# Performance work log

Hardware: AMD Instinct MI355X
Metric: run time of the kernel (lower is better)

Reference implementation:

```python
import jax, jax.numpy as jnp
import numpy as np

N_NODES = 50000
N_EDGES = 800000
N_RELS = 20
N_BASES = 8


def setup_inputs() -> dict:
    key = jax.random.key(0)
    ks = jax.random.split(key, 12)
    s = 0.05  # keep activations well-scaled through summed messages
    return {
        "src": jax.random.randint(ks[0], (N_EDGES,), 0, N_NODES),
        "dst": jax.random.randint(ks[1], (N_EDGES,), 0, N_NODES),
        "etype": jax.random.randint(ks[2], (N_EDGES,), 0, N_RELS),
        "num_nodes": N_NODES,
        "basis0": jax.random.normal(ks[3], (N_BASES, 1, 128), jnp.float32) * s,
        "wcomp0": jax.random.normal(ks[4], (N_RELS, N_BASES), jnp.float32),
        "bias0": jax.random.normal(ks[5], (128,), jnp.float32) * s,
        "basis1": jax.random.normal(ks[6], (N_BASES, 128, 128), jnp.float32) * s,
        "wcomp1": jax.random.normal(ks[7], (N_RELS, N_BASES), jnp.float32),
        "bias1": jax.random.normal(ks[8], (128,), jnp.float32) * s,
        "lin_w": jax.random.normal(ks[9], (128, 64), jnp.float32) * s,
        "lin_b": jax.random.normal(ks[10], (64,), jnp.float32) * s,
    }


def _relgraphconv(h, basis, w_comp, bias, src, dst, etype, num_nodes, relu):
    # Basis decomposition: W[r] = sum_b w_comp[r,b] * basis[b]  -> [R, in, out]
    W = jnp.einsum("rb,bio->rio", w_comp, basis)
    # Project every node under every relation once: [N, R, out]
    proj = jnp.einsum("ni,rio->nro", h, W)
    # Per-edge message = h[src] @ W[etype]  (gather, irregular access)
    msg = proj[src, etype]                       # [E, out]
    # Sum-aggregate messages into destination nodes (DGL fn.sum)
    agg = jax.ops.segment_sum(msg, dst, num_segments=num_nodes)
    out = agg + bias
    return jax.nn.relu(out) if relu else out


def reference(src, dst, etype, num_nodes, basis0, wcomp0, bias0,
              basis1, wcomp1, bias1, lin_w, lin_b):
    # Embedder.forward: h starts as ones [N, 1]
    h = jnp.ones((num_nodes, 1), jnp.float32)
    h = _relgraphconv(h, basis0, wcomp0, bias0, src, dst, etype, num_nodes, True)
    h = _relgraphconv(h, basis1, wcomp1, bias1, src, dst, etype, num_nodes, True)
    # conv_output=False -> final layer is plain Linear
    return h @ lin_w + lin_b
```

## Files before the change

### kernel.cpp

```cpp
#include <hip/hip_runtime.h>
#include <hip/hip_bf16.h>

#define NN 50000
#define NE 800000
#define NR 20
#define NB 8
#define D  128
#define DO 64
#define NT 782
#define NBKT (NT*1280)
#define NSB 978

typedef __attribute__((ext_vector_type(8))) short short8;
typedef __attribute__((ext_vector_type(4))) float f32x4;

__device__ inline unsigned short f2bf(float f) {
    __hip_bfloat16 h = __float2bfloat16(f);
    return *reinterpret_cast<unsigned short*>(&h);
}
__device__ inline float bf2f(unsigned short u) {
    unsigned x = ((unsigned)u) << 16;
    float f;
    __builtin_memcpy(&f, &x, 4);
    return f;
}


__global__ __launch_bounds__(1024) void k_wh(
        const float* __restrict__ basis0, const float* __restrict__ wcomp0,
        const float* __restrict__ basis1, const float* __restrict__ wcomp1,
        const float* __restrict__ lin_w,
        const int* __restrict__ dst, const int* __restrict__ et,
        float* __restrict__ W0, unsigned short* __restrict__ W1b,
        unsigned short* __restrict__ linWb, int* __restrict__ cnt2) {
    int b = blockIdx.x;
    if (b < 40) {
        int idx = b * 1024 + threadIdx.x;
        if (idx < NR * D) {
            int r = idx / D, o = idx % D;
            float a = 0.f;
            #pragma unroll
            for (int bb = 0; bb < NB; bb++) a += wcomp0[r * NB + bb] * basis0[bb * D + o];
            W0[idx] = a;
        }
        if (idx < 16 * 64) {
            int lane = idx & 63, fr = idx >> 6;
            int kc = fr >> 2, nt = fr & 3;
            int i0 = kc * 32 + (lane >> 4) * 8;
            int o = nt * 16 + (lane & 15);
            short8 v;
            #pragma unroll
            for (int e = 0; e < 8; e++) v[e] = (short)f2bf(lin_w[(i0 + e) * DO + o]);
            *((short8*)linWb + idx) = v;
        }
        {
            int lane = idx & 63;
            int cb   = (idx >> 6) & 7;
            int kc   = (idx >> 9) & 3;
            int rel  = idx >> 11;
            float wc[NB];
            #pragma unroll
            for (int bb = 0; bb < NB; bb++) wc[bb] = wcomp1[rel * NB + bb];
            int o  = cb * 16 + (lane & 15);
            int i0 = kc * 32 + (lane >> 4) * 8;
            short8 v;
            #pragma unroll
            for (int e = 0; e < 8; e++) {
                int i = i0 + e;
                float a = 0.f;
                #pragma unroll
                for (int bb = 0; bb < NB; bb++) a += wc[bb] * basis1[(bb * D + i) * D + o];
                v[e] = (short)f2bf(a);
            }
            *((short8*)W1b + idx) = v;
        }
    } else {
        int i = (b - 40) * 1024 + threadIdx.x;
        if (i < NE) {
            int d = dst[i];
            int key = (d >> 6) * 1280 + et[i] * 64 + (d & 63);
            atomicAdd(&cnt2[key], 1);
        }
    }
}

__global__ __launch_bounds__(1024) void k_scan1(const int* __restrict__ cnt2,
                                                int* __restrict__ boff2,
                                                int* __restrict__ bsum,
                                                int* __restrict__ scancnt) {
    __shared__ int ws[16];
    __shared__ int lastf;
    int t = threadIdx.x, lane = t & 63, wv = t >> 6;
    int i = blockIdx.x * 1024 + t;
    int v = (i < NBKT) ? cnt2[i] : 0;
    int inc = v;
    for (int dd = 1; dd < 64; dd <<= 1) {
        int u = __shfl_up(inc, dd);
        if (lane >= dd) inc += u;
    }
    if (lane == 63) ws[wv] = inc;
    __syncthreads();
    if (t == 0) { int a = 0; for (int j = 0; j < 16; j++) { int x = ws[j]; ws[j] = a; a += x; } }
    __syncthreads();
    int ex = ws[wv] + inc - v;
    if (i < NBKT) boff2[i] = ex;
    if (t == 1023) {
        bsum[blockIdx.x] = ex + v;
        __threadfence();
        int done = atomicAdd(scancnt, 1);
        lastf = (done == (int)gridDim.x - 1);
    }
    __syncthreads();
    if (!lastf) return;
    int v2 = (t < NSB) ? atomicAdd(&bsum[t], 0) : 0;
    int inc2 = v2;
    for (int dd = 1; dd < 64; dd <<= 1) {
        int u = __shfl_up(inc2, dd);
        if (lane >= dd) inc2 += u;
    }
    __syncthreads();
    if (lane == 63) ws[wv] = inc2;
    __syncthreads();
    if (t == 0) { int a = 0; for (int j = 0; j < 16; j++) { int x = ws[j]; ws[j] = a; a += x; } }
    __syncthreads();
    if (t < NSB) bsum[t] = ws[wv] + inc2 - v2;
}

__global__ __launch_bounds__(1024) void k_mid(
        int* __restrict__ boff2, const int* __restrict__ bsum,
        int* __restrict__ gcur2, const int* __restrict__ cnt2,
        const float* __restrict__ W0, const float* __restrict__ bias0,
        unsigned short* __restrict__ h1b) {
    __shared__ float cs[NR * 64];
    __shared__ float w0s[NR * D];
    int t = threadIdx.x, b = blockIdx.x;
    int i = b * 1024 + t;
    if (i < NBKT) {
        int f = boff2[i] + bsum[i >> 10];
        boff2[i] = f;
        gcur2[i] = f;
    }
    if (i == 0) boff2[NBKT] = NE;
    if (b < NT) {
        for (int j = t; j < NR * 64; j += 1024) cs[j] = (float)cnt2[b * 1280 + j];
        for (int j = t; j < NR * D; j += 1024) w0s[j] = W0[j];
        __syncthreads();
        int nl = t >> 4, cg = t & 15;
        int n = b * 64 + nl;
        if (n < NN) {
            float a[8];
            #pragma unroll
            for (int j = 0; j < 8; j++) a[j] = bias0[cg * 8 + j];
            for (int r = 0; r < NR; r++) {
                float c = cs[r * 64 + nl];
                #pragma unroll
                for (int j = 0; j < 8; j++) a[j] += c * w0s[r * D + cg * 8 + j];
            }
            short8 o;
            #pragma unroll
            for (int j = 0; j < 8; j++) o[j] = (short)f2bf(fmaxf(a[j], 0.f));
            *((short8*)(h1b + n * D + cg * 8)) = o;
        }
    }
}

__global__ __launch_bounds__(1024) void k_scatter(
        const int* __restrict__ src, const int* __restrict__ dst,
        const int* __restrict__ et, int* __restrict__ gcur2,
        unsigned short* __restrict__ epack) {
    int i = blockIdx.x * 1024 + threadIdx.x;
    if (i < NE) {
        int d = dst[i];
        int key = (d >> 6) * 1280 + et[i] * 64 + (d & 63);
        int pos = atomicAdd(&gcur2[key], 1);
        epack[pos] = (unsigned short)src[i];
    }
}

__global__ __launch_bounds__(512, 2) void k_mega(
        const unsigned short* __restrict__ epack, const int* __restrict__ boff2,
        const unsigned short* __restrict__ h1b,
        const unsigned short* __restrict__ W1b,
        const unsigned short* __restrict__ linWb,
        const float* __restrict__ bias1, const float* __restrict__ lin_b,
        float* __restrict__ out) {
    __shared__ __align__(16) char lds[17408 + 16384];
    __shared__ unsigned short ooffs[1282];
    __shared__ unsigned short epk[2048];

    short8* Raw8 = (short8*)lds;
    short8* Sl8  = (short8*)(lds + 17408);

    int t = threadIdx.x, tile = blockIdx.x;
    int wv = t >> 6, lane = t & 63;
    int le = t >> 3, lp = t & 7;
    int dl = t >> 3, cg = t & 7;
    int row = lane & 15, gg = lane >> 4;

    int kbase = tile * 1280;
    int tb = boff2[kbase];
    for (int i = t; i < 1281; i += 512)
        ooffs[i] = (unsigned short)(boff2[kbase + i] - tb);
    __syncthreads();
    int nE = min((int)ooffs[1280], 2048);
    for (int i = t; i < nE; i += 512) epk[i] = epack[tb + i];
    __syncthreads();

    f32x4 acc[4];
    #pragma unroll
    for (int j = 0; j < 4; j++) acc[j] = (f32x4){0.f, 0.f, 0.f, 0.f};

    for (int r = 0; r < NR; r++) {
        int rbase = ooffs[r * 64];
        int cnt = ooffs[r * 64 + 64] - rbase;
        if (cnt == 0) continue;

        const short8* Wg8 = (const short8*)W1b + r * 2048;
        short8 breg[4];
        #pragma unroll
        for (int kc = 0; kc < 4; kc++) breg[kc] = Wg8[(kc * 8 + wv) * 64 + lane];

        float s[16];
        #pragma unroll
        for (int k = 0; k < 16; k++) s[k] = 0.f;
        int o0 = ooffs[r * 64 + dl] - rbase;
        int o1 = ooffs[r * 64 + dl + 1] - rbase;
        int nc = (cnt + 63) >> 6;

        for (int c = 0; c < nc; c++) {
            int cb0 = c * 64, m = min(64, cnt - cb0);
            if (c > 0) __syncthreads();
            if (le < m) {
                int node = epk[rbase + cb0 + le];
                const short8* hp = (const short8*)(h1b + (size_t)node * D) + lp * 2;
                Raw8[le * 17 + lp * 2]     = hp[0];
                Raw8[le * 17 + lp * 2 + 1] = hp[1];
            }
            __syncthreads();
            int lo = max(o0 - cb0, 0), hi = min(o1 - cb0, m);
            for (int p = lo; p < hi; p++) {
                short8 w0 = Raw8[p * 17 + 2 * cg];
                short8 w1 = Raw8[p * 17 + 2 * cg + 1];
                #pragma unroll
                for (int k = 0; k < 8; k++) {
                    s[k]     += bf2f((unsigned short)w0[k]);
                    s[8 + k] += bf2f((unsigned short)w1[k]);
                }
            }
        }
        short8 p0, p1;
        #pragma unroll
        for (int k = 0; k < 8; k++) {
            p0[k] = (short)f2bf(s[k]);
            p1[k] = (short)f2bf(s[8 + k]);
        }
        Sl8[dl * 16 + ((cg * 2)     ^ (dl & 15))] = p0;
        Sl8[dl * 16 + ((cg * 2 + 1) ^ (dl & 15))] = p1;
        __syncthreads();
        #pragma unroll
        for (int rb = 0; rb < 4; rb++) {
            int arow = rb * 16 + row;
            #pragma unroll
            for (int kc = 0; kc < 4; kc++) {
                short8 a = Sl8[arow * 16 + ((kc * 4 + gg) ^ (arow & 15))];
                acc[rb] = __builtin_amdgcn_mfma_f32_16x16x32_bf16(a, breg[kc], acc[rb], 0, 0, 0);
            }
        }
    }

    __syncthreads();
    unsigned short* Af = (unsigned short*)lds;
    #pragma unroll
    for (int rb = 0; rb < 4; rb++) {
        #pragma unroll
        for (int reg = 0; reg < 4; reg++) {
            int rr = rb * 16 + gg * 4 + reg;
            int col = wv * 16 + row;
            Af[rr * 136 + col] = f2bf(fmaxf(acc[rb][reg] + bias1[col], 0.f));
        }
    }
    __syncthreads();
    {
        int rb = wv & 3;
        int nt0 = (wv >> 2) * 2, nt1 = nt0 + 1;
        f32x4 ao0 = (f32x4){0.f, 0.f, 0.f, 0.f};
        f32x4 ao1 = (f32x4){0.f, 0.f, 0.f, 0.f};
        #pragma unroll
        for (int kc = 0; kc < 4; kc++) {
            short8 a = *(const short8*)(Af + (rb * 16 + row) * 136 + kc * 32 + gg * 8);
            short8 b0 = *((const short8*)linWb + (kc * 4 + nt0) * 64 + lane);
            short8 b1 = *((const short8*)linWb + (kc * 4 + nt1) * 64 + lane);
            ao0 = __builtin_amdgcn_mfma_f32_16x16x32_bf16(a, b0, ao0, 0, 0, 0);
            ao1 = __builtin_amdgcn_mfma_f32_16x16x32_bf16(a, b1, ao1, 0, 0, 0);
        }
        float lb0 = lin_b[nt0 * 16 + row];
        float lb1 = lin_b[nt1 * 16 + row];
        #pragma unroll
        for (int reg = 0; reg < 4; reg++) {
            int d = tile * 64 + rb * 16 + gg * 4 + reg;
            if (d < NN) {
                out[d * DO + nt0 * 16 + row] = ao0[reg] + lb0;
                out[d * DO + nt1 * 16 + row] = ao1[reg] + lb1;
            }
        }
    }
}

extern "C" void kernel_launch(void* const* d_in, const int* in_sizes, int n_in,
                              void* d_out, int out_size, void* d_ws, size_t ws_size,
                              hipStream_t stream) {
    const int*   src    = (const int*)d_in[0];
    const int*   dst    = (const int*)d_in[1];
    const int*   et     = (const int*)d_in[2];
    const float* basis0 = (const float*)d_in[4];
    const float* wcomp0 = (const float*)d_in[5];
    const float* bias0  = (const float*)d_in[6];
    const float* basis1 = (const float*)d_in[7];
    const float* wcomp1 = (const float*)d_in[8];
    const float* bias1  = (const float*)d_in[9];
    const float* lin_w  = (const float*)d_in[10];
    const float* lin_b  = (const float*)d_in[11];
    float* out = (float*)d_out;

    char* ws = (char*)d_ws;
    int*            cnt2    = (int*)           (ws + 0);
    int*            bsum    = (int*)           (ws + 4003840);
    int*            scancnt = (int*)           (ws + 4007752);
    int*            boff2   = (int*)           (ws + 4007808);
    int*            gcur2   = (int*)           (ws + 8011712);
    float*          W0      = (float*)         (ws + 12015616);
    unsigned short* W1b     = (unsigned short*)(ws + 12025856);
    unsigned short* h1b     = (unsigned short*)(ws + 12681216);
    unsigned short* epack   = (unsigned short*)(ws + 25481216);
    unsigned short* linWb   = (unsigned short*)(ws + 28681216);

    hipMemsetAsync(ws, 0, 4007756, stream);

    k_wh<<<NT + 40, 1024, 0, stream>>>(basis0, wcomp0, basis1, wcomp1, lin_w,
                                       dst, et, W0, W1b, linWb, cnt2);
    k_scan1<<<NSB, 1024, 0, stream>>>(cnt2, boff2, bsum, scancnt);
    k_mid<<<NSB, 1024, 0, stream>>>(boff2, bsum, gcur2, cnt2, W0, bias0, h1b);
    k_scatter<<<NT, 1024, 0, stream>>>(src, dst, et, gcur2, epack);
    k_mega<<<NT, 512, 0, stream>>>(epack, boff2, h1b, W1b, linWb,
                                   bias1, lin_b, out);
}
```

Before: 212.0 us.

## Split decoupled scan into separate kernels and fuse layer-0 compute with scatter

Replaces the last-block-done scan (atomic counter plus threadfence) with three kernels: a block-local scan, a single-block scan of the block sums, and an offset-fixup kernel. The layer-0 node feature computation moves from the fixup kernel into the scatter kernel as extra blocks, so it runs alongside the edge scatter. The edge-count blocks are reordered ahead of the weight-prep blocks in the first kernel. This removes the atomic and fence synchronisation but adds one kernel launch.

```diff
diff --git a/kernel.cpp b/kernel.cpp
--- a/kernel.cpp
+++ b/kernel.cpp
@@ -27,69 +27,67 @@
 
 
 __global__ __launch_bounds__(1024) void k_wh(
+        const int* __restrict__ dst, const int* __restrict__ et,
         const float* __restrict__ basis0, const float* __restrict__ wcomp0,
         const float* __restrict__ basis1, const float* __restrict__ wcomp1,
         const float* __restrict__ lin_w,
-        const int* __restrict__ dst, const int* __restrict__ et,
-        float* __restrict__ W0, unsigned short* __restrict__ W1b,
-        unsigned short* __restrict__ linWb, int* __restrict__ cnt2) {
+        int* __restrict__ cnt2, float* __restrict__ W0,
+        unsigned short* __restrict__ W1b, unsigned short* __restrict__ linWb) {
     int b = blockIdx.x;
-    if (b < 40) {
-        int idx = b * 1024 + threadIdx.x;
-        if (idx < NR * D) {
-            int r = idx / D, o = idx % D;
-            float a = 0.f;
-            #pragma unroll
-            for (int bb = 0; bb < NB; bb++) a += wcomp0[r * NB + bb] * basis0[bb * D + o];
-            W0[idx] = a;
-        }
-        if (idx < 16 * 64) {
-            int lane = idx & 63, fr = idx >> 6;
-            int kc = fr >> 2, nt = fr & 3;
-            int i0 = kc * 32 + (lane >> 4) * 8;
-            int o = nt * 16 + (lane & 15);
-            short8 v;
-            #pragma unroll
-            for (int e = 0; e < 8; e++) v[e] = (short)f2bf(lin_w[(i0 + e) * DO + o]);
-            *((short8*)linWb + idx) = v;
-        }
-        {
-            int lane = idx & 63;
-            int cb   = (idx >> 6) & 7;
-            int kc   = (idx >> 9) & 3;
-            int rel  = idx >> 11;
-            float wc[NB];
-            #pragma unroll
-            for (int bb = 0; bb < NB; bb++) wc[bb] = wcomp1[rel * NB + bb];
-            int o  = cb * 16 + (lane & 15);
-            int i0 = kc * 32 + (lane >> 4) * 8;
-            short8 v;
-            #pragma unroll
-            for (int e = 0; e < 8; e++) {
-                int i = i0 + e;
-                float a = 0.f;
-                #pragma unroll
-                for (int bb = 0; bb < NB; bb++) a += wc[bb] * basis1[(bb * D + i) * D + o];
-                v[e] = (short)f2bf(a);
-            }
-            *((short8*)W1b + idx) = v;
-        }
-    } else {
-        int i = (b - 40) * 1024 + threadIdx.x;
+    if (b < NT) {
+        int i = b * 1024 + threadIdx.x;
         if (i < NE) {
             int d = dst[i];
             int key = (d >> 6) * 1280 + et[i] * 64 + (d & 63);
             atomicAdd(&cnt2[key], 1);
         }
+        return;
+    }
+    int idx = (b - NT) * 1024 + threadIdx.x;
+    if (idx < NR * D) {
+        int r = idx / D, o = idx % D;
+        float a = 0.f;
+        #pragma unroll
+        for (int bb = 0; bb < NB; bb++) a += wcomp0[r * NB + bb] * basis0[bb * D + o];
+        W0[idx] = a;
+    }
+    if (idx < 16 * 64) {
+        int lane = idx & 63, fr = idx >> 6;
+        int kc = fr >> 2, nt = fr & 3;
+        int i0 = kc * 32 + (lane >> 4) * 8;
+        int o = nt * 16 + (lane & 15);
+        short8 v;
+        #pragma unroll
+        for (int e = 0; e < 8; e++) v[e] = (short)f2bf(lin_w[(i0 + e) * DO + o]);
+        *((short8*)linWb + idx) = v;
+    }
+    if (idx < NR * 4 * 8 * 64) {
+        int lane = idx & 63;
+        int cb   = (idx >> 6) & 7;
+        int kc   = (idx >> 9) & 3;
+        int rel  = idx >> 11;
+        float wc[NB];
+        #pragma unroll
+        for (int bb = 0; bb < NB; bb++) wc[bb] = wcomp1[rel * NB + bb];
+        int o  = cb * 16 + (lane & 15);
+        int i0 = kc * 32 + (lane >> 4) * 8;
+        short8 v;
+        #pragma unroll
+        for (int e = 0; e < 8; e++) {
+            int i = i0 + e;
+            float a = 0.f;
+            #pragma unroll
+            for (int bb = 0; bb < NB; bb++) a += wc[bb] * basis1[(bb * D + i) * D + o];
+            v[e] = (short)f2bf(a);
+        }
+        *((short8*)W1b + idx) = v;
     }
 }
 
 __global__ __launch_bounds__(1024) void k_scan1(const int* __restrict__ cnt2,
                                                 int* __restrict__ boff2,
-                                                int* __restrict__ bsum,
-                                                int* __restrict__ scancnt) {
+                                                int* __restrict__ bsum) {
     __shared__ int ws[16];
-    __shared__ int lastf;
     int t = threadIdx.x, lane = t & 63, wv = t >> 6;
     int i = blockIdx.x * 1024 + t;
     int v = (i < NBKT) ? cnt2[i] : 0;
@@ -104,76 +102,75 @@
     __syncthreads();
     int ex = ws[wv] + inc - v;
     if (i < NBKT) boff2[i] = ex;
-    if (t == 1023) {
-        bsum[blockIdx.x] = ex + v;
-        __threadfence();
-        int done = atomicAdd(scancnt, 1);
-        lastf = (done == (int)gridDim.x - 1);
-    }
-    __syncthreads();
-    if (!lastf) return;
-    int v2 = (t < NSB) ? atomicAdd(&bsum[t], 0) : 0;
-    int inc2 = v2;
+    if (t == 1023) bsum[blockIdx.x] = ex + v;
+}
+
+__global__ __launch_bounds__(1024) void k_scan2(int* __restrict__ bsum) {
+    __shared__ int ws[16];
+    int t = threadIdx.x, lane = t & 63, wv = t >> 6;
+    int v = (t < NSB) ? bsum[t] : 0;
+    int inc = v;
     for (int dd = 1; dd < 64; dd <<= 1) {
-        int u = __shfl_up(inc2, dd);
-        if (lane >= dd) inc2 += u;
-    }
-    __syncthreads();
-    if (lane == 63) ws[wv] = inc2;
+        int u = __shfl_up(inc, dd);
+        if (lane >= dd) inc += u;
+    }
+    if (lane == 63) ws[wv] = inc;
     __syncthreads();
     if (t == 0) { int a = 0; for (int j = 0; j < 16; j++) { int x = ws[j]; ws[j] = a; a += x; } }
     __syncthreads();
-    if (t < NSB) bsum[t] = ws[wv] + inc2 - v2;
-}
-
-__global__ __launch_bounds__(1024) void k_mid(
-        int* __restrict__ boff2, const int* __restrict__ bsum,
-        int* __restrict__ gcur2, const int* __restrict__ cnt2,
-        const float* __restrict__ W0, const float* __restrict__ bias0,
-        unsigned short* __restrict__ h1b) {
-    __shared__ float cs[NR * 64];
-    __shared__ float w0s[NR * D];
-    int t = threadIdx.x, b = blockIdx.x;
-    int i = b * 1024 + t;
+    if (t < NSB) bsum[t] = ws[wv] + inc - v;
+}
+
+__global__ __launch_bounds__(1024) void k_scan3(int* __restrict__ boff2,
+                                                const int* __restrict__ bsum,
+                                                int* __restrict__ gcur2) {
+    int i = blockIdx.x * 1024 + threadIdx.x;
     if (i < NBKT) {
         int f = boff2[i] + bsum[i >> 10];
         boff2[i] = f;
         gcur2[i] = f;
     }
     if (i == 0) boff2[NBKT] = NE;
-    if (b < NT) {
-        for (int j = t; j < NR * 64; j += 1024) cs[j] = (float)cnt2[b * 1280 + j];
-        for (int j = t; j < NR * D; j += 1024) w0s[j] = W0[j];
-        __syncthreads();
-        int nl = t >> 4, cg = t & 15;
-        int n = b * 64 + nl;
-        if (n < NN) {
-            float a[8];
-            #pragma unroll
-            for (int j = 0; j < 8; j++) a[j] = bias0[cg * 8 + j];
-            for (int r = 0; r < NR; r++) {
-                float c = cs[r * 64 + nl];
-                #pragma unroll
-                for (int j = 0; j < 8; j++) a[j] += c * w0s[r * D + cg * 8 + j];
-            }
-            short8 o;
-            #pragma unroll
-            for (int j = 0; j < 8; j++) o[j] = (short)f2bf(fmaxf(a[j], 0.f));
-            *((short8*)(h1b + n * D + cg * 8)) = o;
-        }
-    }
-}
-
-__global__ __launch_bounds__(1024) void k_scatter(
+}
+
+__global__ __launch_bounds__(1024) void k_sh(
         const int* __restrict__ src, const int* __restrict__ dst,
         const int* __restrict__ et, int* __restrict__ gcur2,
-        unsigned short* __restrict__ epack) {
-    int i = blockIdx.x * 1024 + threadIdx.x;
-    if (i < NE) {
-        int d = dst[i];
-        int key = (d >> 6) * 1280 + et[i] * 64 + (d & 63);
-        int pos = atomicAdd(&gcur2[key], 1);
-        epack[pos] = (unsigned short)src[i];
+        unsigned short* __restrict__ epack,
+        const int* __restrict__ cnt2, const float* __restrict__ W0,
+        const float* __restrict__ bias0, unsigned short* __restrict__ h1b) {
+    int b = blockIdx.x, t = threadIdx.x;
+    if (b < NT) {
+        int i = b * 1024 + t;
+        if (i < NE) {
+            int d = dst[i];
+            int key = (d >> 6) * 1280 + et[i] * 64 + (d & 63);
+            int pos = atomicAdd(&gcur2[key], 1);
+            epack[pos] = (unsigned short)src[i];
+        }
+        return;
+    }
+    __shared__ float cs[NR * 64];
+    __shared__ float w0s[NR * D];
+    int tile = b - NT;
+    for (int j = t; j < NR * 64; j += 1024) cs[j] = (float)cnt2[tile * 1280 + j];
+    for (int j = t; j < NR * D; j += 1024) w0s[j] = W0[j];
+    __syncthreads();
+    int nl = t >> 4, cg = t & 15;
+    int n = tile * 64 + nl;
+    if (n < NN) {
+        float a[8];
+        #pragma unroll
+        for (int j = 0; j < 8; j++) a[j] = bias0[cg * 8 + j];
+        for (int r = 0; r < NR; r++) {
+            float c = cs[r * 64 + nl];
+            #pragma unroll
+            for (int j = 0; j < 8; j++) a[j] += c * w0s[r * D + cg * 8 + j];
+        }
+        short8 o;
+        #pragma unroll
+        for (int j = 0; j < 8; j++) o[j] = (short)f2bf(fmaxf(a[j], 0.f));
+        *((short8*)(h1b + n * D + cg * 8)) = o;
     }
 }
 
@@ -325,7 +322,6 @@
     char* ws = (char*)d_ws;
     int*            cnt2    = (int*)           (ws + 0);
     int*            bsum    = (int*)           (ws + 4003840);
-    int*            scancnt = (int*)           (ws + 4007752);
     int*            boff2   = (int*)           (ws + 4007808);
     int*            gcur2   = (int*)           (ws + 8011712);
     float*          W0      = (float*)         (ws + 12015616);
@@ -334,13 +330,15 @@
     unsigned short* epack   = (unsigned short*)(ws + 25481216);
     unsigned short* linWb   = (unsigned short*)(ws + 28681216);
 
-    hipMemsetAsync(ws, 0, 4007756, stream);
-
-    k_wh<<<NT + 40, 1024, 0, stream>>>(basis0, wcomp0, basis1, wcomp1, lin_w,
-                                       dst, et, W0, W1b, linWb, cnt2);
-    k_scan1<<<NSB, 1024, 0, stream>>>(cnt2, boff2, bsum, scancnt);
-    k_mid<<<NSB, 1024, 0, stream>>>(boff2, bsum, gcur2, cnt2, W0, bias0, h1b);
-    k_scatter<<<NT, 1024, 0, stream>>>(src, dst, et, gcur2, epack);
+    hipMemsetAsync(ws, 0, 4003840, stream);
+
+    k_wh<<<NT + 40, 1024, 0, stream>>>(dst, et, basis0, wcomp0, basis1, wcomp1,
+                                       lin_w, cnt2, W0, W1b, linWb);
+    k_scan1<<<NSB, 1024, 0, stream>>>(cnt2, boff2, bsum);
+    k_scan2<<<1, 1024, 0, stream>>>(bsum);
+    k_scan3<<<NSB, 1024, 0, stream>>>(boff2, bsum, gcur2);
+    k_sh<<<NT * 2, 1024, 0, stream>>>(src, dst, et, gcur2, epack,
+                                      cnt2, W0, bias0, h1b);
     k_mega<<<NT, 512, 0, stream>>>(epack, boff2, h1b, W1b, linWb,
                                    bias1, lin_b, out);
 }
```

New measurement: 190.0 us. -10.4%, faster.
